# Performance work log

Hardware: AMD Instinct MI355X
Metric: run time of the kernel (lower is better)

The kernel has to match this reference:

```python
import jax, jax.numpy as jnp
import numpy as np

EPS = 1e-5  # BatchNorm2d default eps


def _deform_conv(x, offset, W_def, b_def, K):
    # torchvision.ops.DeformConv2d, stride=1, dilation=1, padding=K//2, groups=1
    B, C, H, W = x.shape
    KK = K * K
    pad = K // 2
    # offset channels ordered (y, x) per kernel tap: [B, KK, 2, H, W]
    off = offset.reshape(B, KK, 2, H, W)
    ky = (jnp.arange(KK) // K).astype(x.dtype)
    kx = (jnp.arange(KK) % K).astype(x.dtype)
    base_y = jnp.arange(H, dtype=x.dtype)[None, :, None] - pad + ky[:, None, None]  # [KK,H,1]
    base_x = jnp.arange(W, dtype=x.dtype)[None, None, :] - pad + kx[:, None, None]  # [KK,1,W]
    py = off[:, :, 0] + base_y[None]  # [B,KK,H,W] sampling rows
    px = off[:, :, 1] + base_x[None]  # [B,KK,H,W] sampling cols
    y0 = jnp.floor(py)
    x0 = jnp.floor(px)
    wy = py - y0
    wx = px - x0
    xf = x.reshape(B, C, H * W)

    def corner(iy, ix, w):
        valid = ((iy >= 0) & (iy < H) & (ix >= 0) & (ix < W)).astype(x.dtype)
        idx = jnp.clip(iy, 0, H - 1).astype(jnp.int32) * W + jnp.clip(ix, 0, W - 1).astype(jnp.int32)
        g = jnp.take_along_axis(xf, idx.reshape(B, 1, KK * H * W), axis=2)
        return g.reshape(B, C, KK, H, W) * (w * valid)[:, None]

    sampled = (corner(y0, x0, (1 - wy) * (1 - wx))
               + corner(y0, x0 + 1, (1 - wy) * wx)
               + corner(y0 + 1, x0, wy * (1 - wx))
               + corner(y0 + 1, x0 + 1, wy * wx))  # [B,C,KK,H,W]
    out = jnp.einsum('bckhw,ock->bohw', sampled, W_def.reshape(W_def.shape[0], C, KK))
    return out + b_def[None, :, None, None]


def reference(x, W_off, b_off, W_def, b_def, W_cat, b_cat, gamma, beta):
    K = W_def.shape[-1]
    # 3x3 offset-generating conv, padding=1
    offset = jax.lax.conv_general_dilated(
        x, W_off, (1, 1), ((1, 1), (1, 1)),
        dimension_numbers=('NCHW', 'OIHW', 'NCHW')) + b_off[None, :, None, None]
    y1 = _deform_conv(x, offset, W_def, b_def, K)
    # 1x1 conv
    y = jnp.einsum('bchw,oc->bohw', y1, W_cat) + b_cat[None, :, None, None]
    # BatchNorm2d in training mode (batch statistics, biased var)
    mean = y.mean(axis=(0, 2, 3))
    var = y.var(axis=(0, 2, 3))
    yn = (y - mean[None, :, None, None]) * jax.lax.rsqrt(var + EPS)[None, :, None, None]
    out = jax.nn.relu(gamma[None, :, None, None] * yn + beta[None, :, None, None])
    return out + x


def setup_inputs() -> dict:
    key = jax.random.key(0)
    ks = jax.random.split(key, 5)
    B, C, H, W, K = 4, 64, 192, 192, 3
    return {
        'x': jax.random.normal(ks[0], (B, C, H, W), dtype=jnp.float32),
        'W_off': jax.random.normal(ks[1], (2 * K * K, C, 3, 3), dtype=jnp.float32) * 0.02,
        'b_off': jnp.zeros((2 * K * K,), dtype=jnp.float32),
        'W_def': jax.random.normal(ks[2], (C, C, K, K), dtype=jnp.float32) * (1.0 / np.sqrt(C * K * K)),
        'b_def': jnp.zeros((C,), dtype=jnp.float32),
        'W_cat': jax.random.normal(ks[3], (C, C), dtype=jnp.float32) * (1.0 / np.sqrt(C)),
        'b_cat': jnp.zeros((C,), dtype=jnp.float32),
        'gamma': jnp.ones((C,), dtype=jnp.float32),
        'beta': jnp.zeros((C,), dtype=jnp.float32),
    }
```

## Files before the change

### kernel.cpp

```cpp
#include <hip/hip_runtime.h>
#include <math.h>

constexpr int Hh  = 192;
constexpr int Ww  = 192;
constexpr int HWp = Hh * Ww;
constexpr int Cc  = 64;
constexpr int Bb  = 4;
constexpr int KK  = 9;
constexpr int OFFC = 18;
constexpr int PXB = 32;
constexpr int NBPX = HWp / PXB;
constexpr int KSD = (Cc * KK) / 32;
constexpr int KSC = Cc / 32;
constexpr int NIT = KK * PXB;
constexpr int SLOTS = 64;
constexpr int XT_COLS = PXB + 2;
constexpr int XT_ITEMS = 3 * XT_COLS;

constexpr int NXP = Bb * (HWp / 64);
constexpr int NWP = (4 * KSD * 64 * 8 + 4 * KSC * 64 * 8 + 2 * KSD * 64 * 8) / 256;
constexpr int NZP = (2 * Cc * SLOTS / 4) / 256;

using bf16x8 = __attribute__((ext_vector_type(8))) short;
using f32x4  = __attribute__((ext_vector_type(4))) float;
using f32x2  = __attribute__((ext_vector_type(2))) float;

static __device__ __forceinline__ unsigned short f2bf(float f) {
    unsigned int u = __float_as_uint(f);
    u += 0x7fff + ((u >> 16) & 1);
    return (unsigned short)(u >> 16);
}
static __device__ __forceinline__ float bf2f(unsigned short u) {
    return __uint_as_float((unsigned)u << 16);
}

__global__ __launch_bounds__(256)
void k_prep(const float* __restrict__ x, const float* __restrict__ Wdef,
            const float* __restrict__ Wcat, const float* __restrict__ Woff,
            unsigned short* __restrict__ xcl, unsigned short* __restrict__ Fd,
            unsigned short* __restrict__ Fc, unsigned short* __restrict__ Fo,
            float* __restrict__ psum) {
    __shared__ unsigned int wtile[64][32];
    const int bid = blockIdx.x;
    const int t = threadIdx.x;
    if (bid < NXP) {
        int b   = bid / (HWp / 64);
        int px0 = (bid % (HWp / 64)) * 64;
        #pragma unroll
        for (int r = 0; r < 4; ++r) {
            int cc = r * 16 + (t >> 4), px4 = (t & 15) * 4;
            float4 v = *(const float4*)(x + ((size_t)b * Cc + cc) * HWp + px0 + px4);
            unsigned lo  = (unsigned)f2bf(v.x) | ((unsigned)f2bf(v.y) << 16);
            unsigned hi2 = (unsigned)f2bf(v.z) | ((unsigned)f2bf(v.w) << 16);
            unsigned e = (unsigned)(cc & 31);
            wtile[cc][((unsigned)(px4 >> 1)    ) ^ e] = lo;
            wtile[cc][((unsigned)(px4 >> 1) + 1) ^ e] = hi2;
        }
        __syncthreads();
        #pragma unroll
        for (int r = 0; r < 4; ++r) {
            int pxl = r * 16 + (t >> 4), c4l = (t & 15) * 4;
            int hsel = (pxl & 1) * 16;
            unsigned w0 = wtile[c4l + 0][(unsigned)(pxl >> 1) ^ (unsigned)((c4l + 0) & 31)];
            unsigned w1 = wtile[c4l + 1][(unsigned)(pxl >> 1) ^ (unsigned)((c4l + 1) & 31)];
            unsigned w2 = wtile[c4l + 2][(unsigned)(pxl >> 1) ^ (unsigned)((c4l + 2) & 31)];
            unsigned w3 = wtile[c4l + 3][(unsigned)(pxl >> 1) ^ (unsigned)((c4l + 3) & 31)];
            ushort4 u;
            u.x = (unsigned short)(w0 >> hsel);
            u.y = (unsigned short)(w1 >> hsel);
            u.z = (unsigned short)(w2 >> hsel);
            u.w = (unsigned short)(w3 >> hsel);
            *(ushort4*)(xcl + ((size_t)b * HWp + px0 + pxl) * Cc + c4l) = u;
        }
    } else if (bid < NXP + NWP) {
        int i = (bid - NXP) * 256 + t;
        if (i < 4 * KSD * 64 * 8) {
            int r = i & 7, lane = (i >> 3) & 63, ks = (i >> 9) % KSD, ot = (i >> 9) / KSD;
            int o  = ot * 16 + (lane & 15);
            int kp = ks * 32 + ((lane >> 4) << 3) + r;
            int kk = kp >> 6, c = kp & 63;
            Fd[i] = f2bf(Wdef[o * (Cc * KK) + c * KK + kk]);
        }
        int j = i - 4 * KSD * 64 * 8;
        if (j >= 0 && j < 4 * KSC * 64 * 8) {
            int r = j & 7, lane = (j >> 3) & 63, ks = (j >> 9) & 1, ot = j >> 10;
            int o = ot * 16 + (lane & 15);
            int c = ks * 32 + ((lane >> 4) << 3) + r;
            Fc[j] = f2bf(Wcat[o * Cc + c]);
        }
        int m = j - 4 * KSC * 64 * 8;
        if (m >= 0 && m < 2 * KSD * 64 * 8) {
            int r = m & 7, lane = (m >> 3) & 63, ks = (m >> 9) % KSD, ot = (m >> 9) / KSD;
            int o  = ot * 16 + (lane & 15);
            int kp = ks * 32 + ((lane >> 4) << 3) + r;
            int kk = kp >> 6, c = kp & 63;
            Fo[m] = (o < OFFC) ? f2bf(Woff[o * (Cc * KK) + c * KK + kk]) : 0;
        }
    } else {
        int j = (bid - NXP - NWP) * 256 + t;
        float4 z = {0.f, 0.f, 0.f, 0.f};
        ((float4*)psum)[j] = z;
    }
}

__global__ __launch_bounds__(256, 3)
void k_fused(const unsigned short* __restrict__ xcl,
             const unsigned short* __restrict__ Fo, const float* __restrict__ boff,
             const unsigned short* __restrict__ Fd, const float* __restrict__ bdef,
             const unsigned short* __restrict__ Fc, const float* __restrict__ bcat,
             unsigned short* __restrict__ y, float* __restrict__ psum) {
    __shared__ __align__(16) unsigned char s_buf[PXB * Cc * KK * 2];
    __shared__ __align__(16) unsigned char s_y1[PXB * Cc * 2];
    __shared__ float s_off[PXB][OFFC];
    __shared__ __align__(16) int s_pp[NIT * 8];

    const int t = threadIdx.x;
    const int lane = t & 63, wv = t >> 6;
    const int klane = (lane >> 4) & 3;
    const int c4 = (lane & 15) * 4;
    int wg = blockIdx.x;
    const int slot = wg & (SLOTS - 1);
    wg = (wg & 7) * (Bb * NBPX / 8) + (wg >> 3);
    const int b   = wg / NBPX;
    const int px0 = (wg % NBPX) * PXB;
    const int h   = px0 / Ww;
    const int w0  = px0 % Ww;
    const unsigned short* xb = xcl + (size_t)b * HWp * Cc;

    #pragma unroll
    for (int it = 0; it < 7; ++it) {
        int item = it * 16 + wv * 4 + klane;
        if (item < XT_ITEMS) {
            int ry = item / XT_COLS, cx = item - ry * XT_COLS;
            int row = h + ry - 1, col = w0 + cx - 1;
            ushort4 u = {0, 0, 0, 0};
            if (row >= 0 && row < Hh && col >= 0 && col < Ww)
                u = *(const ushort4*)(xb + (size_t)(row * Ww + col) * Cc + c4);
            unsigned addr = (unsigned)item * 128
                          + (((unsigned)c4 * 2) ^ (((unsigned)item & 7) << 4));
            *(ushort4*)(s_buf + addr) = u;
        }
    }
    __syncthreads();

    {
        const int oto = wv >> 1, pxt0 = wv & 1;
        const int pxv = (lane & 15) + pxt0 * 16;
        f32x4 a = {0.f, 0.f, 0.f, 0.f};
        const bf16x8* Bo = (const bf16x8*)Fo + (size_t)oto * KSD * 64;
        #pragma unroll
        for (int ks = 0; ks < KSD; ++ks) {
            const int kk = ks >> 1;
            const int ky = kk / 3, kx = kk % 3;
            int row_l = ky * XT_COLS + pxv + kx;
            unsigned c0b = (unsigned)(((ks & 1) * 32 + klane * 8) * 2);
            unsigned addr = (unsigned)row_l * 128 + (c0b ^ (((unsigned)row_l & 7) << 4));
            bf16x8 af = *(const bf16x8*)(s_buf + addr);
            a = __builtin_amdgcn_mfma_f32_16x16x32_bf16(af, Bo[ks * 64 + lane], a, 0, 0, 0);
        }
        int oc = oto * 16 + (lane & 15);
        if (oc < OFFC) {
            float bv = boff[oc];
            #pragma unroll
            for (int r = 0; r < 4; ++r)
                s_off[pxt0 * 16 + klane * 4 + r][oc] = a[r] + bv;
        }
    }
    __syncthreads();

    for (int i = t; i < NIT; i += 256) {
        int kk = i >> 5, pxl = i & 31;
        int ky = (kk * 11) >> 5, kx = kk - ky * 3;
        float py  = s_off[pxl][kk * 2]     + (float)(h - 1 + ky);
        float pxf = s_off[pxl][kk * 2 + 1] + (float)(w0 + pxl - 1 + kx);
        float fy0 = floorf(py), fx0 = floorf(pxf);
        float wy = py - fy0, wx = pxf - fx0;
        int iy0 = (int)fy0, ix0 = (int)fx0, iy1 = iy0 + 1, ix1 = ix0 + 1;
        float v00 = (iy0 >= 0 && iy0 < Hh && ix0 >= 0 && ix0 < Ww) ? 1.f : 0.f;
        float v01 = (iy0 >= 0 && iy0 < Hh && ix1 >= 0 && ix1 < Ww) ? 1.f : 0.f;
        float v10 = (iy1 >= 0 && iy1 < Hh && ix0 >= 0 && ix0 < Ww) ? 1.f : 0.f;
        float v11 = (iy1 >= 0 && iy1 < Hh && ix1 >= 0 && ix1 < Ww) ? 1.f : 0.f;
        int cy0 = min(max(iy0, 0), Hh - 1), cy1 = min(max(iy1, 0), Hh - 1);
        int cx0 = min(max(ix0, 0), Ww - 1), cx1 = min(max(ix1, 0), Ww - 1);
        int* pp = &s_pp[i * 8];
        pp[0] = (cy0 * Ww + cx0) * (Cc * 2);
        pp[1] = (cy0 * Ww + cx1) * (Cc * 2);
        pp[2] = (cy1 * Ww + cx0) * (Cc * 2);
        pp[3] = (cy1 * Ww + cx1) * (Cc * 2);
        pp[4] = __float_as_int((1.f - wy) * (1.f - wx) * v00);
        pp[5] = __float_as_int((1.f - wy) * wx * v01);
        pp[6] = __float_as_int(wy * (1.f - wx) * v10);
        pp[7] = __float_as_int(wy * wx * v11);
    }
    __syncthreads();

    const unsigned char* xbB = (const unsigned char*)xb + (size_t)c4 * 2;
    #pragma unroll 6
    for (int it = 0; it < NIT / 16; ++it) {
        int item = it * 16 + wv * 4 + klane;
        int kk = item >> 5, pxl = item & 31;
        const int* pp = &s_pp[item * 8];
        int4   idx = *(const int4*)pp;
        float4 wt  = *(const float4*)(pp + 4);
        ushort4 u00 = *(const ushort4*)(xbB + idx.x);
        ushort4 u01 = *(const ushort4*)(xbB + idx.y);
        ushort4 u10 = *(const ushort4*)(xbB + idx.z);
        ushort4 u11 = *(const ushort4*)(xbB + idx.w);
        f32x2 lo00 = {bf2f(u00.x), bf2f(u00.y)}, hi00 = {bf2f(u00.z), bf2f(u00.w)};
        f32x2 lo01 = {bf2f(u01.x), bf2f(u01.y)}, hi01 = {bf2f(u01.z), bf2f(u01.w)};
        f32x2 lo10 = {bf2f(u10.x), bf2f(u10.y)}, hi10 = {bf2f(u10.z), bf2f(u10.w)};
        f32x2 lo11 = {bf2f(u11.x), bf2f(u11.y)}, hi11 = {bf2f(u11.z), bf2f(u11.w)};
        f32x2 vlo = wt.x * lo00 + wt.y * lo01 + wt.z * lo10 + wt.w * lo11;
        f32x2 vhi = wt.x * hi00 + wt.y * hi01 + wt.z * hi10 + wt.w * hi11;
        ushort4 o4;
        o4.x = f2bf(vlo[0]); o4.y = f2bf(vlo[1]); o4.z = f2bf(vhi[0]); o4.w = f2bf(vhi[1]);
        unsigned addr = (unsigned)pxl * (Cc * KK * 2)
                      + ((((unsigned)(kk * 64 + c4)) * 2) ^ ((unsigned)(pxl & 7) << 4));
        *(ushort4*)(s_buf + addr) = o4;
    }
    __syncthreads();

    const int ot = wv;
    const unsigned swzA = (unsigned)(lane & 7) << 4;
    const unsigned rA0  = (unsigned)(lane & 15) * (Cc * KK * 2);
    const unsigned rA1  = rA0 + 16u * (Cc * KK * 2);
    f32x4 acc0 = {0.f, 0.f, 0.f, 0.f}, acc1 = {0.f, 0.f, 0.f, 0.f};
    const bf16x8* Bd = (const bf16x8*)Fd + (size_t)ot * KSD * 64;
    #pragma unroll 3
    for (int ks = 0; ks < KSD; ++ks) {
        unsigned cb = ((unsigned)(ks * 64 + klane * 16)) ^ swzA;
        bf16x8 a0 = *(const bf16x8*)(s_buf + rA0 + cb);
        bf16x8 a1 = *(const bf16x8*)(s_buf + rA1 + cb);
        bf16x8 bd = Bd[ks * 64 + lane];
        acc0 = __builtin_amdgcn_mfma_f32_16x16x32_bf16(a0, bd, acc0, 0, 0, 0);
        acc1 = __builtin_amdgcn_mfma_f32_16x16x32_bf16(a1, bd, acc1, 0, 0, 0);
    }
    const int o = ot * 16 + (lane & 15);
    {
        float bv = bdef[o];
        unsigned colb = (unsigned)o * 2;
        #pragma unroll
        for (int r = 0; r < 4; ++r) {
            int row0 = klane * 4 + r, row1 = row0 + 16;
            unsigned sw = (unsigned)(row0 & 7) << 4;
            *(unsigned short*)(s_y1 + row0 * (Cc * 2) + (colb ^ sw)) = f2bf(acc0[r] + bv);
            *(unsigned short*)(s_y1 + row1 * (Cc * 2) + (colb ^ sw)) = f2bf(acc1[r] + bv);
        }
    }
    __syncthreads();

    f32x4 c0 = {0.f, 0.f, 0.f, 0.f}, c1 = {0.f, 0.f, 0.f, 0.f};
    const bf16x8* Bc = (const bf16x8*)Fc + (size_t)ot * KSC * 64;
    const unsigned rY0 = (unsigned)(lane & 15) * (Cc * 2);
    const unsigned rY1 = rY0 + 16u * (Cc * 2);
    #pragma unroll
    for (int ks = 0; ks < KSC; ++ks) {
        unsigned cb = ((unsigned)(ks * 64 + klane * 16)) ^ swzA;
        bf16x8 a0 = *(const bf16x8*)(s_y1 + rY0 + cb);
        bf16x8 a1 = *(const bf16x8*)(s_y1 + rY1 + cb);
        bf16x8 bc = Bc[ks * 64 + lane];
        c0 = __builtin_amdgcn_mfma_f32_16x16x32_bf16(a0, bc, c0, 0, 0, 0);
        c1 = __builtin_amdgcn_mfma_f32_16x16x32_bf16(a1, bc, c1, 0, 0, 0);
    }

    float vals[8];
    {
        float bcv = bcat[o];
        #pragma unroll
        for (int r = 0; r < 4; ++r) { vals[r] = c0[r] + bcv; vals[4 + r] = c1[r] + bcv; }
        float s1 = 0.f, s2 = 0.f;
        #pragma unroll
        for (int j = 0; j < 8; ++j) { s1 += vals[j]; s2 += vals[j] * vals[j]; }
        s1 += __shfl_xor(s1, 16); s1 += __shfl_xor(s1, 32);
        s2 += __shfl_xor(s2, 16); s2 += __shfl_xor(s2, 32);
        if (klane == 0) {
            atomicAdd(&psum[o * SLOTS + slot], s1);
            atomicAdd(&psum[Cc * SLOTS + o * SLOTS + slot], s2);
        }
    }

    __syncthreads();
    {
        unsigned orow = (unsigned)o * (PXB * 4);
        unsigned sw   = (unsigned)(o & 7) << 4;
        #pragma unroll
        for (int r = 0; r < 4; ++r) {
            int p0 = klane * 4 + r, p1 = p0 + 16;
            *(float*)(s_buf + orow + (((unsigned)p0 * 4) ^ sw)) = vals[r];
            *(float*)(s_buf + orow + (((unsigned)p1 * 4) ^ sw)) = vals[4 + r];
        }
    }
    __syncthreads();
    unsigned short* yb = y + (size_t)b * Cc * HWp + px0;
    #pragma unroll
    for (int it = 0; it < 2; ++it) {
        int oo = it * 32 + (t >> 3), pxq = t & 7;
        float4 v = *(const float4*)(s_buf + (unsigned)oo * (PXB * 4)
                                    + (((unsigned)pxq * 16) ^ ((unsigned)(oo & 7) << 4)));
        ushort4 u;
        u.x = f2bf(v.x); u.y = f2bf(v.y); u.z = f2bf(v.z); u.w = f2bf(v.w);
        *(ushort4*)(yb + (size_t)oo * HWp + pxq * 4) = u;
    }
}

__global__ __launch_bounds__(256)
void k_apply(const unsigned short* __restrict__ y, const float4* __restrict__ x,
             const float* __restrict__ psum, const float* __restrict__ gamma,
             const float* __restrict__ beta, float4* __restrict__ out) {
    __shared__ float smv[2];
    const int t = threadIdx.x;
    const int idx = blockIdx.x * 256 + t;
    const int c = (blockIdx.x * 1024 / HWp) % Cc;
    if (t < 64) {
        float s1 = psum[c * SLOTS + t];
        float s2 = psum[Cc * SLOTS + c * SLOTS + t];
        #pragma unroll
        for (int d = 1; d < 64; d <<= 1) {
            s1 += __shfl_xor(s1, d);
            s2 += __shfl_xor(s2, d);
        }
        if (t == 0) {
            float n = (float)(Bb * HWp);
            float mean = s1 / n;
            float var  = s2 / n - mean * mean;
            smv[0] = mean;
            smv[1] = 1.0f / sqrtf(var + 1e-5f);
        }
    }
    __syncthreads();
    float mean = smv[0], inv = smv[1];
    float g = gamma[c], bt = beta[c];
    ushort4 yv = *(const ushort4*)(y + (size_t)idx * 4);
    float4 xv = x[idx], o;
    o.x = fmaxf(g * ((bf2f(yv.x) - mean) * inv) + bt, 0.f) + xv.x;
    o.y = fmaxf(g * ((bf2f(yv.y) - mean) * inv) + bt, 0.f) + xv.y;
    o.z = fmaxf(g * ((bf2f(yv.z) - mean) * inv) + bt, 0.f) + xv.z;
    o.w = fmaxf(g * ((bf2f(yv.w) - mean) * inv) + bt, 0.f) + xv.w;
    out[idx] = o;
}

extern "C" void kernel_launch(void* const* d_in, const int* in_sizes, int n_in,
                              void* d_out, int out_size, void* d_ws, size_t ws_size,
                              hipStream_t stream) {
    const float* x     = (const float*)d_in[0];
    const float* Woff  = (const float*)d_in[1];
    const float* boff  = (const float*)d_in[2];
    const float* Wdef  = (const float*)d_in[3];
    const float* bdef  = (const float*)d_in[4];
    const float* Wcat  = (const float*)d_in[5];
    const float* bcat  = (const float*)d_in[6];
    const float* gamma = (const float*)d_in[7];
    const float* beta  = (const float*)d_in[8];
    float* out = (float*)d_out;

    float* ws    = (float*)d_ws;
    float* psum  = ws;
    unsigned short* y16 = (unsigned short*)(psum + 2 * Cc * SLOTS);
    unsigned short* Fd  = y16 + (size_t)Bb * Cc * HWp;
    unsigned short* Fc  = Fd + 4 * KSD * 64 * 8;
    unsigned short* Fo  = Fc + 4 * KSC * 64 * 8;
    unsigned short* xcl = Fo + 2 * KSD * 64 * 8;

    k_prep<<<dim3(NXP + NWP + NZP), dim3(256), 0, stream>>>(x, Wdef, Wcat, Woff,
                                                            xcl, Fd, Fc, Fo, psum);
    k_fused<<<dim3(Bb * NBPX), dim3(256), 0, stream>>>(xcl, Fo, boff, Fd, bdef, Fc, bcat, y16, psum);
    k_apply<<<dim3(Bb * Cc * HWp / 4 / 256), dim3(256), 0, stream>>>(
        y16, (const float4*)x, psum, gamma, beta, (float4*)out);
}
```

Before: 207.2 us.

## Halve pixel tile per block to double occupancy and store y directly

Reduces the per-block pixel tile from 32 to 16 pixels, which halves LDS use and raises the occupancy hint from 3 to 6 blocks per CU. The offset-conv MFMA now runs on only two waves, and each wave issues one MFMA chain instead of two for the deformable and 1x1 convs. The LDS transpose before writing y is removed; each lane writes 4 consecutive bf16 pixels straight to global memory. In exchange, more blocks must reload the overlapping halo rows and weights, per-wave MFMA work is smaller, and the direct stores are narrower (8-byte) writes.

```diff
diff --git a/kernel.cpp b/kernel.cpp
--- a/kernel.cpp
+++ b/kernel.cpp
@@ -8,7 +8,7 @@
 constexpr int Bb  = 4;
 constexpr int KK  = 9;
 constexpr int OFFC = 18;
-constexpr int PXB = 32;
+constexpr int PXB = 16;
 constexpr int NBPX = HWp / PXB;
 constexpr int KSD = (Cc * KK) / 32;
 constexpr int KSC = Cc / 32;
@@ -103,7 +103,7 @@
     }
 }
 
-__global__ __launch_bounds__(256, 3)
+__global__ __launch_bounds__(256, 6)
 void k_fused(const unsigned short* __restrict__ xcl,
              const unsigned short* __restrict__ Fo, const float* __restrict__ boff,
              const unsigned short* __restrict__ Fd, const float* __restrict__ bdef,
@@ -128,7 +128,7 @@
     const unsigned short* xb = xcl + (size_t)b * HWp * Cc;
 
     #pragma unroll
-    for (int it = 0; it < 7; ++it) {
+    for (int it = 0; it < 4; ++it) {
         int item = it * 16 + wv * 4 + klane;
         if (item < XT_ITEMS) {
             int ry = item / XT_COLS, cx = item - ry * XT_COLS;
@@ -143,9 +143,9 @@
     }
     __syncthreads();
 
-    {
-        const int oto = wv >> 1, pxt0 = wv & 1;
-        const int pxv = (lane & 15) + pxt0 * 16;
+    if (wv < 2) {
+        const int oto = wv;
+        const int pxv = lane & 15;
         f32x4 a = {0.f, 0.f, 0.f, 0.f};
         const bf16x8* Bo = (const bf16x8*)Fo + (size_t)oto * KSD * 64;
         #pragma unroll
@@ -163,13 +163,14 @@
             float bv = boff[oc];
             #pragma unroll
             for (int r = 0; r < 4; ++r)
-                s_off[pxt0 * 16 + klane * 4 + r][oc] = a[r] + bv;
-        }
-    }
-    __syncthreads();
-
-    for (int i = t; i < NIT; i += 256) {
-        int kk = i >> 5, pxl = i & 31;
+                s_off[klane * 4 + r][oc] = a[r] + bv;
+        }
+    }
+    __syncthreads();
+
+    if (t < NIT) {
+        int i = t;
+        int kk = i >> 4, pxl = i & 15;
         int ky = (kk * 11) >> 5, kx = kk - ky * 3;
         float py  = s_off[pxl][kk * 2]     + (float)(h - 1 + ky);
         float pxf = s_off[pxl][kk * 2 + 1] + (float)(w0 + pxl - 1 + kx);
@@ -195,10 +196,10 @@
     __syncthreads();
 
     const unsigned char* xbB = (const unsigned char*)xb + (size_t)c4 * 2;
-    #pragma unroll 6
+    #pragma unroll 3
     for (int it = 0; it < NIT / 16; ++it) {
         int item = it * 16 + wv * 4 + klane;
-        int kk = item >> 5, pxl = item & 31;
+        int kk = item >> 4, pxl = item & 15;
         const int* pp = &s_pp[item * 8];
         int4   idx = *(const int4*)pp;
         float4 wt  = *(const float4*)(pp + 4);
@@ -222,18 +223,15 @@
 
     const int ot = wv;
     const unsigned swzA = (unsigned)(lane & 7) << 4;
-    const unsigned rA0  = (unsigned)(lane & 15) * (Cc * KK * 2);
-    const unsigned rA1  = rA0 + 16u * (Cc * KK * 2);
-    f32x4 acc0 = {0.f, 0.f, 0.f, 0.f}, acc1 = {0.f, 0.f, 0.f, 0.f};
+    const unsigned rA = (unsigned)(lane & 15) * (Cc * KK * 2);
+    f32x4 acc = {0.f, 0.f, 0.f, 0.f};
     const bf16x8* Bd = (const bf16x8*)Fd + (size_t)ot * KSD * 64;
     #pragma unroll 3
     for (int ks = 0; ks < KSD; ++ks) {
         unsigned cb = ((unsigned)(ks * 64 + klane * 16)) ^ swzA;
-        bf16x8 a0 = *(const bf16x8*)(s_buf + rA0 + cb);
-        bf16x8 a1 = *(const bf16x8*)(s_buf + rA1 + cb);
+        bf16x8 a0 = *(const bf16x8*)(s_buf + rA + cb);
         bf16x8 bd = Bd[ks * 64 + lane];
-        acc0 = __builtin_amdgcn_mfma_f32_16x16x32_bf16(a0, bd, acc0, 0, 0, 0);
-        acc1 = __builtin_amdgcn_mfma_f32_16x16x32_bf16(a1, bd, acc1, 0, 0, 0);
+        acc = __builtin_amdgcn_mfma_f32_16x16x32_bf16(a0, bd, acc, 0, 0, 0);
     }
     const int o = ot * 16 + (lane & 15);
     {
@@ -241,65 +239,41 @@
         unsigned colb = (unsigned)o * 2;
         #pragma unroll
         for (int r = 0; r < 4; ++r) {
-            int row0 = klane * 4 + r, row1 = row0 + 16;
-            unsigned sw = (unsigned)(row0 & 7) << 4;
-            *(unsigned short*)(s_y1 + row0 * (Cc * 2) + (colb ^ sw)) = f2bf(acc0[r] + bv);
-            *(unsigned short*)(s_y1 + row1 * (Cc * 2) + (colb ^ sw)) = f2bf(acc1[r] + bv);
-        }
-    }
-    __syncthreads();
-
-    f32x4 c0 = {0.f, 0.f, 0.f, 0.f}, c1 = {0.f, 0.f, 0.f, 0.f};
+            int row = klane * 4 + r;
+            unsigned sw = (unsigned)(row & 7) << 4;
+            *(unsigned short*)(s_y1 + row * (Cc * 2) + (colb ^ sw)) = f2bf(acc[r] + bv);
+        }
+    }
+    __syncthreads();
+
+    f32x4 cacc = {0.f, 0.f, 0.f, 0.f};
     const bf16x8* Bc = (const bf16x8*)Fc + (size_t)ot * KSC * 64;
-    const unsigned rY0 = (unsigned)(lane & 15) * (Cc * 2);
-    const unsigned rY1 = rY0 + 16u * (Cc * 2);
+    const unsigned rY = (unsigned)(lane & 15) * (Cc * 2);
     #pragma unroll
     for (int ks = 0; ks < KSC; ++ks) {
         unsigned cb = ((unsigned)(ks * 64 + klane * 16)) ^ swzA;
-        bf16x8 a0 = *(const bf16x8*)(s_y1 + rY0 + cb);
-        bf16x8 a1 = *(const bf16x8*)(s_y1 + rY1 + cb);
+        bf16x8 a0 = *(const bf16x8*)(s_y1 + rY + cb);
         bf16x8 bc = Bc[ks * 64 + lane];
-        c0 = __builtin_amdgcn_mfma_f32_16x16x32_bf16(a0, bc, c0, 0, 0, 0);
-        c1 = __builtin_amdgcn_mfma_f32_16x16x32_bf16(a1, bc, c1, 0, 0, 0);
-    }
-
-    float vals[8];
+        cacc = __builtin_amdgcn_mfma_f32_16x16x32_bf16(a0, bc, cacc, 0, 0, 0);
+    }
+
     {
         float bcv = bcat[o];
-        #pragma unroll
-        for (int r = 0; r < 4; ++r) { vals[r] = c0[r] + bcv; vals[4 + r] = c1[r] + bcv; }
+        float vals[4];
+        #pragma unroll
+        for (int r = 0; r < 4; ++r) vals[r] = cacc[r] + bcv;
         float s1 = 0.f, s2 = 0.f;
         #pragma unroll
-        for (int j = 0; j < 8; ++j) { s1 += vals[j]; s2 += vals[j] * vals[j]; }
+        for (int j = 0; j < 4; ++j) { s1 += vals[j]; s2 += vals[j] * vals[j]; }
         s1 += __shfl_xor(s1, 16); s1 += __shfl_xor(s1, 32);
         s2 += __shfl_xor(s2, 16); s2 += __shfl_xor(s2, 32);
         if (klane == 0) {
             atomicAdd(&psum[o * SLOTS + slot], s1);
             atomicAdd(&psum[Cc * SLOTS + o * SLOTS + slot], s2);
         }
-    }
-
-    __syncthreads();
-    {
-        unsigned orow = (unsigned)o * (PXB * 4);
-        unsigned sw   = (unsigned)(o & 7) << 4;
-        #pragma unroll
-        for (int r = 0; r < 4; ++r) {
-            int p0 = klane * 4 + r, p1 = p0 + 16;
-            *(float*)(s_buf + orow + (((unsigned)p0 * 4) ^ sw)) = vals[r];
-            *(float*)(s_buf + orow + (((unsigned)p1 * 4) ^ sw)) = vals[4 + r];
-        }
-    }
-    __syncthreads();
-    unsigned short* yb = y + (size_t)b * Cc * HWp + px0;
-    #pragma unroll
-    for (int it = 0; it < 2; ++it) {
-        int oo = it * 32 + (t >> 3), pxq = t & 7;
-        float4 v = *(const float4*)(s_buf + (unsigned)oo * (PXB * 4)
-                                    + (((unsigned)pxq * 16) ^ ((unsigned)(oo & 7) << 4)));
         ushort4 u;
-        u.x = f2bf(v.x); u.y = f2bf(v.y); u.z = f2bf(v.z); u.w = f2bf(v.w);
-        *(ushort4*)(yb + (size_t)oo * HWp + pxq * 4) = u;
+        u.x = f2bf(vals[0]); u.y = f2bf(vals[1]); u.z = f2bf(vals[2]); u.w = f2bf(vals[3]);
+        *(ushort4*)(y + ((size_t)(b * Cc + o)) * HWp + px0 + klane * 4) = u;
     }
 }
 
```

New measurement: 224.6 us. 1.08x slower.
